# Kernel optimization log

Hardware: AMD Instinct MI355X
Metric: run time of the kernel (lower is better)

The kernel has to match this reference:

```python
import jax, jax.numpy as jnp
import numpy as np

# --- Mamba2Simple hyperparams (from module defaults + headdim=64 hardcode) ---
D_MODEL = 512
D_STATE = 128
EXPAND = 2
HEADDIM = 64
D_INNER = EXPAND * D_MODEL          # 1024
NHEADS = D_INNER // HEADDIM         # 16
NGROUPS = 1
D_CONV = 4
CHUNK = 128                          # SSD chunk length
CONV_DIM = D_INNER + 2 * NGROUPS * D_STATE          # 1280
D_IN_PROJ = 2 * D_INNER + 2 * NGROUPS * D_STATE + NHEADS  # 2320
B_SZ, SEQ = 4, 4096
EPS = 1e-5


def setup_inputs() -> dict:
    key = jax.random.key(0)
    ks = jax.random.split(key, 8)
    x = jax.random.normal(ks[0], (B_SZ, SEQ, D_MODEL), jnp.float32)
    W_in = jax.random.normal(ks[1], (D_IN_PROJ, D_MODEL), jnp.float32) * 0.02
    conv_w = jax.random.normal(ks[2], (CONV_DIM, D_CONV), jnp.float32) * 0.1
    conv_b = jnp.zeros((CONV_DIM,), jnp.float32)
    # dt_bias = inverse-softplus of dt in [1e-3, 0.1] (mamba2 init)
    dt = jax.random.uniform(ks[3], (NHEADS,), jnp.float32, 1e-3, 0.1)
    dt_bias = jnp.log(jnp.expm1(dt))
    A_log = jnp.log(jax.random.uniform(ks[4], (NHEADS,), jnp.float32, 1.0, 16.0))
    D = jnp.ones((NHEADS,), jnp.float32)
    norm_w = jnp.ones((D_INNER,), jnp.float32)
    W_out = jax.random.normal(ks[5], (D_MODEL, D_INNER), jnp.float32) * 0.02
    return dict(x=x, W_in=W_in, conv_w=conv_w, conv_b=conv_b, dt_bias=dt_bias,
                A_log=A_log, D=D, norm_w=norm_w, W_out=W_out)


def _causal_conv(x, w, b):
    """Depthwise causal conv1d. x: (b,l,c), w: (c,K), b: (c,)."""
    lhs = x.transpose(0, 2, 1)          # (b,c,l)
    rhs = w[:, None, :]                  # (c,1,K) depthwise
    out = jax.lax.conv_general_dilated(lhs, rhs, (1,), [(D_CONV - 1, 0)],
                                       feature_group_count=CONV_DIM)
    return out.transpose(0, 2, 1) + b


def _segsum(a):
    """a: (..., T) -> (..., T, T) with out[i,j] = sum_{j<k<=i} a[k], -inf above diag."""
    T = a.shape[-1]
    cs = jnp.cumsum(a, -1)
    seg = cs[..., :, None] - cs[..., None, :]
    mask = jnp.tril(jnp.ones((T, T), bool))
    return jnp.where(mask, seg, -jnp.inf)


def _ssd(X, A, B, C):
    """Chunked SSD scan (ssd_minimal_discrete).
    X: (b,l,h,p) (= dt*x), A: (b,l,h) (= dt*A, negative), B,C: (b,l,n). ngroups=1.
    """
    b, l, h, p = X.shape
    c = l // CHUNK
    Xc = X.reshape(b, c, CHUNK, h, p)
    Ac = A.reshape(b, c, CHUNK, h).transpose(0, 3, 1, 2)   # (b,h,c,q)
    Bc = B.reshape(b, c, CHUNK, -1)                         # (b,c,q,n)
    Cc = C.reshape(b, c, CHUNK, -1)
    A_cs = jnp.cumsum(Ac, -1)                               # (b,h,c,q)
    # intra-chunk (quadratic) part
    Lmat = jnp.exp(_segsum(Ac))                             # (b,h,c,q,q) causal decay
    Y_diag = jnp.einsum('bcqn,bcsn,bhcqs,bcshp->bcqhp', Cc, Bc, Lmat, Xc)
    # per-chunk final states
    decay_states = jnp.exp(A_cs[..., -1:] - A_cs)           # (b,h,c,q)
    states = jnp.einsum('bcqn,bhcq,bcqhp->bchpn', Bc, decay_states, Xc)
    # inter-chunk recurrence (initial state = 0)
    A_last = jnp.pad(A_cs[..., -1], ((0, 0), (0, 0), (1, 0)))  # (b,h,c+1)
    decay_chunk = jnp.exp(_segsum(A_last))                     # (b,h,c+1,c+1)
    states = jnp.concatenate([jnp.zeros_like(states[:, :1]), states], axis=1)
    new_states = jnp.einsum('bhzc,bchpn->bzhpn', decay_chunk, states)
    prev_states = new_states[:, :-1]                           # (b,c,h,p,n)
    Y_off = jnp.einsum('bcqn,bchpn,bhcq->bcqhp', Cc, prev_states, jnp.exp(A_cs))
    return (Y_diag + Y_off).reshape(b, l, h, p)


def _forward(x, W_in, conv_w, conv_b, dt_bias, A_log, D, norm_w, W_out):
    bsz, L, _ = x.shape
    zxbcdt = x @ W_in.T                                   # (b,l,2320)
    z = zxbcdt[..., :D_INNER]
    xBC = zxbcdt[..., D_INNER:D_INNER + CONV_DIM]
    dt = jax.nn.softplus(zxbcdt[..., -NHEADS:] + dt_bias)  # (b,l,h)
    xBC = jax.nn.silu(_causal_conv(xBC, conv_w, conv_b))
    xs = xBC[..., :D_INNER].reshape(bsz, L, NHEADS, HEADDIM)
    Bm = xBC[..., D_INNER:D_INNER + D_STATE]               # (b,l,n)
    Cm = xBC[..., D_INNER + D_STATE:]                      # (b,l,n)
    A = -jnp.exp(A_log)                                    # (h,)
    y = _ssd(xs * dt[..., None], dt * A, Bm, Cm)           # (b,l,h,p)
    y = y + D[None, None, :, None] * xs                    # D skip
    y = y.reshape(bsz, L, D_INNER)
    # gated RMSNorm (norm_before_gate=False): rmsnorm(y * silu(z)) * w
    g = y * jax.nn.silu(z)
    g = g * jax.lax.rsqrt(jnp.mean(g * g, -1, keepdims=True) + EPS) * norm_w
    return x + g @ W_out.T                                 # residual add


def reference(x, W_in, conv_w, conv_b, dt_bias, A_log, D, norm_w, W_out):
    return _forward(x, W_in, conv_w, conv_b, dt_bias, A_log, D, norm_w, W_out)
```

## Files before the change

kernel.cpp:

```cpp
#include <hip/hip_runtime.h>
#include <hip/hip_bf16.h>

typedef __hip_bfloat16 bf16;
typedef __attribute__((ext_vector_type(8))) __bf16 bf16x8;
typedef __attribute__((ext_vector_type(4))) float f32x4;

constexpr int BSZ = 4, SEQ = 4096, DMODEL = 512;
constexpr int DSTATE = 128, HEADDIM = 64, DINNER = 1024, NHEADS = 16, CHUNK = 128;
constexpr int CONVDIM = DINNER + 2 * DSTATE;
constexpr int DINPROJ = 2 * DINNER + 2 * DSTATE + NHEADS;
constexpr int NPAD = 2432;
constexpr int MTOT = BSZ * SEQ;
constexpr int NCHUNK = SEQ / CHUNK;

constexpr size_t OFF_Z    = 0;
constexpr size_t OFF_XBC  = OFF_Z    + (size_t)MTOT * DINNER * 2;
constexpr size_t OFF_DT   = OFF_XBC  + (size_t)MTOT * CONVDIM * 2;
constexpr size_t OFF_XS   = OFF_DT   + (size_t)MTOT * NHEADS * 4;
constexpr size_t OFF_B    = OFF_XS   + (size_t)MTOT * DINNER * 2;
constexpr size_t OFF_C    = OFF_B    + (size_t)MTOT * DSTATE * 2;
constexpr size_t OFF_G    = OFF_C    + (size_t)MTOT * DSTATE * 2;
constexpr size_t OFF_ASUM = OFF_G    + (size_t)BSZ * NCHUNK * CHUNK * CHUNK * 2;
constexpr size_t WS_NEED  = OFF_ASUM + 8192;

static __device__ __forceinline__ float sigmoidf_(float x) { return 1.f / (1.f + __expf(-x)); }
static __device__ __forceinline__ unsigned short f2bf_bits(float f) {
    __hip_bfloat16 h = __float2bfloat16(f);
    return *reinterpret_cast<unsigned short*>(&h);
}
static __device__ __forceinline__ float bfbits2f(unsigned short u) {
    return __bfloat162float(*reinterpret_cast<bf16*>(&u));
}
struct us4 { unsigned short a, b, c, d; };
static __device__ __forceinline__ us4 pack4(const f32x4 v) {
    return { f2bf_bits(v[0]), f2bf_bits(v[1]), f2bf_bits(v[2]), f2bf_bits(v[3]) };
}

__global__ void k_sentinel(float* out) { out[0] = 1.0e9f; }

__global__ __launch_bounds__(256) void k_cast_x(const float* __restrict__ in, bf16* __restrict__ out, int n4) {
    int i = blockIdx.x * 256 + threadIdx.x;
    if (i >= n4) return;
    float4 f = ((const float4*)in)[i];
    us4 v = { f2bf_bits(f.x), f2bf_bits(f.y), f2bf_bits(f.z), f2bf_bits(f.w) };
    ((us4*)out)[i] = v;
}

__global__ __launch_bounds__(256) void k_cast_win(const float* __restrict__ W, bf16* __restrict__ out) {
    int i = blockIdx.x * 256 + threadIdx.x;
    if (i >= NPAD * (DMODEL / 4)) return;
    int row = i / (DMODEL / 4);
    us4 v;
    if (row < DINPROJ) {
        float4 f = ((const float4*)W)[i];
        v = { f2bf_bits(f.x), f2bf_bits(f.y), f2bf_bits(f.z), f2bf_bits(f.w) };
    } else {
        v = { 0, 0, 0, 0 };
    }
    ((us4*)out)[i] = v;
}

typedef const __attribute__((address_space(1))) void* gas_t;
typedef __attribute__((address_space(3))) void* las_t;
static __device__ __forceinline__ void gload_lds16(const void* g, void* l) {
    __builtin_amdgcn_global_load_lds((gas_t)g, (las_t)l, 16, 0, 0);
}

template<int K>
static __device__ __forceinline__ void gemm_core(
    const bf16* __restrict__ A, const bf16* __restrict__ B,
    int m0, int n0, bf16* ldsA, bf16* ldsB, f32x4 acc[4][4])
{
    constexpr int NT = K / 32;
    const int tid = threadIdx.x;
    const int l = tid & 63, w = tid >> 6;
    const int wr = w >> 1, wc = w & 1;
    const int lq = l & 15, lk = l >> 4;

    auto stage = [&](int buf, int t) {
        const int k0 = t * 32;
        #pragma unroll
        for (int i = 0; i < 2; ++i) {
            int q = w * 16 + i * 8 + (l >> 3);
            int p = l & 7;
            int L = p ^ (q & 7);
            int ra = (L >> 2) * 64 + q;
            int ck = L & 3;
            gload_lds16(A + (size_t)(m0 + ra) * K + k0 + ck * 8,
                        ldsA + buf * 4096 + (w * 16 + i * 8) * 64);
            gload_lds16(B + (size_t)(n0 + ra) * K + k0 + ck * 8,
                        ldsB + buf * 4096 + (w * 16 + i * 8) * 64);
        }
    };

    stage(0, 0);
    stage(1, 1);
    for (int t = 0; t < NT; ++t) {
        if (t + 1 < NT) asm volatile("s_waitcnt vmcnt(4)" ::: "memory");
        else            asm volatile("s_waitcnt vmcnt(0)" ::: "memory");
        __builtin_amdgcn_s_barrier();
        __builtin_amdgcn_sched_barrier(0);
        if (t + 2 < NT) stage((t + 2) % 3, t + 2);
        const int buf = t % 3;
        bf16x8 av[4], bv[4];
        #pragma unroll
        for (int f = 0; f < 4; ++f) {
            int ra = wr * 64 + f * 16 + lq;
            int qa = ra & 63, La = (ra >> 6) * 4 + lk, pa = La ^ (qa & 7);
            av[f] = *(const bf16x8*)(ldsA + buf * 4096 + qa * 64 + pa * 8);
            int rb = wc * 64 + f * 16 + lq;
            int qb = rb & 63, Lb = (rb >> 6) * 4 + lk, pb = Lb ^ (qb & 7);
            bv[f] = *(const bf16x8*)(ldsB + buf * 4096 + qb * 64 + pb * 8);
        }
        #pragma unroll
        for (int nf = 0; nf < 4; ++nf)
            #pragma unroll
            for (int mf = 0; mf < 4; ++mf)
                acc[nf][mf] = __builtin_amdgcn_mfma_f32_16x16x32_bf16(bv[nf], av[mf], acc[nf][mf], 0, 0, 0);
    }
}

static __device__ __forceinline__ void swz_block(int& bx, int& by) {
    int gx = gridDim.x;
    int nwg = gx * gridDim.y;
    int wg = by * gx + bx;
    int q = nwg >> 3;
    wg = (wg & 7) * q + (wg >> 3);
    bx = wg % gx; by = wg / gx;
}

__global__ __launch_bounds__(256) void k_gemm_in(
    const bf16* __restrict__ xb, const bf16* __restrict__ Wb,
    const float* __restrict__ dt_bias,
    bf16* __restrict__ z, bf16* __restrict__ xbc, float* __restrict__ dtb)
{
    __shared__ bf16 ldsA[3 * 4096];
    __shared__ bf16 ldsB[3 * 4096];
    int bx = blockIdx.x, by = blockIdx.y;
    swz_block(bx, by);
    const int m0 = by * 128, n0 = bx * 128;
    f32x4 acc[4][4] = {};
    gemm_core<DMODEL>(xb, Wb, m0, n0, ldsA, ldsB, acc);
    const int l = threadIdx.x & 63, w = threadIdx.x >> 6;
    const int wr = w >> 1, wc = w & 1, lq = l & 15, lk = l >> 4;
    const int mg = m0 + wr * 64, ng = n0 + wc * 64;
    if (n0 < DINNER) {
        #pragma unroll
        for (int nf = 0; nf < 4; ++nf)
            #pragma unroll
            for (int mf = 0; mf < 4; ++mf) {
                int n = ng + nf * 16 + lk * 4;
                int m = mg + mf * 16 + lq;
                *(us4*)(z + (size_t)m * DINNER + n) = pack4(acc[nf][mf]);
            }
    } else if (n0 < DINNER + CONVDIM) {
        #pragma unroll
        for (int nf = 0; nf < 4; ++nf)
            #pragma unroll
            for (int mf = 0; mf < 4; ++mf) {
                int n = ng + nf * 16 + lk * 4 - DINNER;
                int m = mg + mf * 16 + lq;
                *(us4*)(xbc + (size_t)m * CONVDIM + n) = pack4(acc[nf][mf]);
            }
    } else {
        #pragma unroll
        for (int nf = 0; nf < 4; ++nf)
            #pragma unroll
            for (int mf = 0; mf < 4; ++mf)
                #pragma unroll
                for (int j = 0; j < 4; ++j) {
                    int n = ng + nf * 16 + lk * 4 + j;
                    int m = mg + mf * 16 + lq;
                    if (n < DINPROJ) {
                        int h = n - (DINNER + CONVDIM);
                        float t = acc[nf][mf][j] + dt_bias[h];
                        dtb[(size_t)m * NHEADS + h] = (t > 20.f) ? t : log1pf(__expf(t));
                    }
                }
    }
}

__global__ __launch_bounds__(256) void k_gemm_out(
    const bf16* __restrict__ gb, const bf16* __restrict__ Wb,
    const float* __restrict__ xres, float* __restrict__ outp)
{
    __shared__ bf16 ldsA[3 * 4096];
    __shared__ bf16 ldsB[3 * 4096];
    int bx = blockIdx.x, by = blockIdx.y;
    swz_block(bx, by);
    const int m0 = by * 128, n0 = bx * 128;
    f32x4 acc[4][4] = {};
    gemm_core<DINNER>(gb, Wb, m0, n0, ldsA, ldsB, acc);
    const int l = threadIdx.x & 63, w = threadIdx.x >> 6;
    const int wr = w >> 1, wc = w & 1, lq = l & 15, lk = l >> 4;
    const int mg = m0 + wr * 64, ng = n0 + wc * 64;
    #pragma unroll
    for (int nf = 0; nf < 4; ++nf)
        #pragma unroll
        for (int mf = 0; mf < 4; ++mf) {
            int n = ng + nf * 16 + lk * 4;
            int m = mg + mf * 16 + lq;
            float4 r = *(const float4*)(xres + (size_t)m * DMODEL + n);
            float4 o = { r.x + acc[nf][mf][0], r.y + acc[nf][mf][1],
                         r.z + acc[nf][mf][2], r.w + acc[nf][mf][3] };
            *(float4*)(outp + (size_t)m * DMODEL + n) = o;
        }
}

constexpr int CTOK = 8;
__global__ __launch_bounds__(320) void k_conv(
    const bf16* __restrict__ xbc, const float* __restrict__ cw, const float* __restrict__ cb,
    bf16* __restrict__ xs, bf16* __restrict__ Bm, bf16* __restrict__ Cm)
{
    const int m0 = blockIdx.x * CTOK;
    const int c4 = threadIdx.x;
    const int c = c4 * 4;
    const int l0 = m0 & 4095;
    float4 cbv = ((const float4*)cb)[c4];
    const float4 w0 = ((const float4*)cw)[c + 0];
    const float4 w1 = ((const float4*)cw)[c + 1];
    const float4 w2 = ((const float4*)cw)[c + 2];
    const float4 w3 = ((const float4*)cw)[c + 3];
    us4 rows[CTOK + 3];
    #pragma unroll
    for (int t = -3; t < CTOK; ++t) {
        int ll = l0 + t;
        if (ll >= 0) rows[t + 3] = *(const us4*)(xbc + (size_t)(m0 + t) * CONVDIM + c);
        else         rows[t + 3] = { 0, 0, 0, 0 };
    }
    #pragma unroll
    for (int t = 0; t < CTOK; ++t) {
        float a0 = cbv.x, a1 = cbv.y, a2 = cbv.z, a3 = cbv.w;
        #pragma unroll
        for (int k = 0; k < 4; ++k) {
            us4 v = rows[t + k];
            a0 += bfbits2f(v.a) * ((const float*)&w0)[k];
            a1 += bfbits2f(v.b) * ((const float*)&w1)[k];
            a2 += bfbits2f(v.c) * ((const float*)&w2)[k];
            a3 += bfbits2f(v.d) * ((const float*)&w3)[k];
        }
        us4 o = { f2bf_bits(a0 * sigmoidf_(a0)), f2bf_bits(a1 * sigmoidf_(a1)),
                  f2bf_bits(a2 * sigmoidf_(a2)), f2bf_bits(a3 * sigmoidf_(a3)) };
        int m = m0 + t;
        if (c < DINNER)               *(us4*)(xs + (size_t)m * DINNER + c) = o;
        else if (c < DINNER + DSTATE) *(us4*)(Bm + (size_t)m * DSTATE + (c - DINNER)) = o;
        else                          *(us4*)(Cm + (size_t)m * DSTATE + (c - DINNER - DSTATE)) = o;
    }
}

__global__ __launch_bounds__(64) void k_gmat(
    const bf16* __restrict__ Cm, const bf16* __restrict__ Bm, bf16* __restrict__ G)
{
    const int bc = blockIdx.z;
    const int q0 = blockIdx.x * 64, s0 = blockIdx.y * 64;
    const int row0 = bc * CHUNK;
    const int l = threadIdx.x;
    const int lq = l & 15, lk = l >> 4;
    f32x4 acc[4][4] = {};
    #pragma unroll
    for (int kc = 0; kc < 4; ++kc) {
        bf16x8 av[4], bv[4];
        #pragma unroll
        for (int f = 0; f < 4; ++f) {
            av[f] = *(const bf16x8*)(Cm + (size_t)(row0 + q0 + f * 16 + lq) * DSTATE + kc * 32 + lk * 8);
            bv[f] = *(const bf16x8*)(Bm + (size_t)(row0 + s0 + f * 16 + lq) * DSTATE + kc * 32 + lk * 8);
        }
        #pragma unroll
        for (int fs = 0; fs < 4; ++fs)
            #pragma unroll
            for (int fq = 0; fq < 4; ++fq)
                acc[fs][fq] = __builtin_amdgcn_mfma_f32_16x16x32_bf16(bv[fs], av[fq], acc[fs][fq], 0, 0, 0);
    }
    #pragma unroll
    for (int fs = 0; fs < 4; ++fs)
        #pragma unroll
        for (int fq = 0; fq < 4; ++fq) {
            int q = q0 + fq * 16 + lq;
            int s = s0 + fs * 16 + lk * 4;
            *(us4*)(G + ((size_t)bc * CHUNK + q) * CHUNK + s) = pack4(acc[fs][fq]);
        }
}

__global__ __launch_bounds__(256) void k_ssd(
    const bf16* __restrict__ xs , const bf16* __restrict__ Bm,
    const float* __restrict__ dtb, const float* __restrict__ A_log,
    const float* __restrict__ Dp, const bf16* __restrict__ G,
    bf16* __restrict__ y, bf16* __restrict__ states, float* __restrict__ asum)
{
    const int h = blockIdx.x, c = blockIdx.y, b = blockIdx.z;
    const int tid = threadIdx.x;
    const int l = tid & 63, w = tid >> 6;
    const int lq = l & 15, lk = l >> 4;
    __shared__ float sa[CHUNK], sdt[CHUNK], sdec[CHUNK];
    __shared__ __bf16 Xt[HEADDIM][136];
    __shared__ __bf16 Bt[DSTATE][136];
    const int row0 = b * SEQ + c * CHUNK;
    const int bc = b * NCHUNK + c;
    const float Ah = -__expf(A_log[h]);
    const float Dh = Dp[h];
    if (tid < CHUNK) {
        float d = dtb[(size_t)(row0 + tid) * NHEADS + h];
        sdt[tid] = d;
        sa[tid] = d * Ah;
    }
    __syncthreads();
    for (int off = 1; off < CHUNK; off <<= 1) {
        float v = 0.f;
        if (tid < CHUNK && tid >= off) v = sa[tid - off];
        __syncthreads();
        if (tid < CHUNK) sa[tid] += v;
        __syncthreads();
    }
    const float alast = sa[CHUNK - 1];
    if (tid < CHUNK) sdec[tid] = __expf(alast - sa[tid]);
    __syncthreads();
    {
        const int s = tid >> 1;
        const float dts = sdt[s];
        #pragma unroll
        for (int li = 0; li < 4; ++li) {
            int p0 = (tid & 1) * 8 + li * 16;
            bf16x8 v = *(const bf16x8*)(xs + (size_t)(row0 + s) * DINNER + h * HEADDIM + p0);
            #pragma unroll
            for (int i = 0; i < 8; ++i) Xt[p0 + i][s] = (__bf16)((float)v[i] * dts);
        }
        #pragma unroll
        for (int li = 0; li < 8; ++li) {
            int n0 = (tid & 1) * 8 + li * 16;
            bf16x8 v = *(const bf16x8*)(Bm + (size_t)(row0 + s) * DSTATE + n0);
            #pragma unroll
            for (int i = 0; i < 8; ++i) Bt[n0 + i][s] = v[i];
        }
    }
    __syncthreads();
    __builtin_amdgcn_s_setprio(1);
    {
        const int q0 = w * 32;
        f32x4 acc[4][2] = {};
        #pragma unroll
        for (int kc = 0; kc < 4; ++kc) {
            const int sbase = kc * 32 + lk * 8;
            bf16x8 av[2];
            #pragma unroll
            for (int fr = 0; fr < 2; ++fr) {
                int q = q0 + fr * 16 + lq;
                bf16x8 g = *(const bf16x8*)(G + ((size_t)bc * CHUNK + q) * CHUNK + sbase);
                float saq = sa[q];
                bf16x8 wv;
                #pragma unroll
                for (int j = 0; j < 8; ++j) {
                    int s = sbase + j;
                    float val = (s <= q) ? __expf(saq - sa[s]) * (float)g[j] : 0.f;
                    wv[j] = (__bf16)val;
                }
                av[fr] = wv;
            }
            #pragma unroll
            for (int pf = 0; pf < 4; ++pf) {
                bf16x8 xv = *(const bf16x8*)&Xt[pf * 16 + lq][sbase];
                #pragma unroll
                for (int fr = 0; fr < 2; ++fr)
                    acc[pf][fr] = __builtin_amdgcn_mfma_f32_16x16x32_bf16(xv, av[fr], acc[pf][fr], 0, 0, 0);
            }
        }
        #pragma unroll
        for (int fr = 0; fr < 2; ++fr)
            #pragma unroll
            for (int pf = 0; pf < 4; ++pf) {
                int q = q0 + fr * 16 + lq;
                int p = pf * 16 + lk * 4;
                size_t idx = (size_t)(row0 + q) * DINNER + h * HEADDIM + p;
                us4 xv4 = *(const us4*)(xs + idx);
                f32x4 a = acc[pf][fr];
                us4 o = { f2bf_bits(a[0] + Dh * bfbits2f(xv4.a)),
                          f2bf_bits(a[1] + Dh * bfbits2f(xv4.b)),
                          f2bf_bits(a[2] + Dh * bfbits2f(xv4.c)),
                          f2bf_bits(a[3] + Dh * bfbits2f(xv4.d)) };
                *(us4*)(y + idx) = o;
            }
    }
    {
        const int n0 = w * 32;
        f32x4 acc[2][4] = {};
        #pragma unroll
        for (int kc = 0; kc < 4; ++kc) {
            const int sbase = kc * 32 + lk * 8;
            bf16x8 xd[4];
            #pragma unroll
            for (int pf = 0; pf < 4; ++pf) {
                bf16x8 xv = *(const bf16x8*)&Xt[pf * 16 + lq][sbase];
                bf16x8 sc;
                #pragma unroll
                for (int j = 0; j < 8; ++j) sc[j] = (__bf16)((float)xv[j] * sdec[sbase + j]);
                xd[pf] = sc;
            }
            #pragma unroll
            for (int nf = 0; nf < 2; ++nf) {
                bf16x8 bb = *(const bf16x8*)&Bt[n0 + nf * 16 + lq][sbase];
                #pragma unroll
                for (int pf = 0; pf < 4; ++pf)
                    acc[nf][pf] = __builtin_amdgcn_mfma_f32_16x16x32_bf16(bb, xd[pf], acc[nf][pf], 0, 0, 0);
            }
        }
        __builtin_amdgcn_s_setprio(0);
        const size_t sb = ((size_t)bc * NHEADS + h) * (HEADDIM * DSTATE);
        #pragma unroll
        for (int nf = 0; nf < 2; ++nf)
            #pragma unroll
            for (int pf = 0; pf < 4; ++pf) {
                int p = pf * 16 + lq;
                int n = n0 + nf * 16 + lk * 4;
                *(us4*)(states + sb + (size_t)p * DSTATE + n) = pack4(acc[nf][pf]);
            }
    }
    if (tid == 0) asum[bc * NHEADS + h] = alast;
}

__global__ __launch_bounds__(256) void k_scan(bf16* __restrict__ states, const float* __restrict__ asum)
{
    const int h = blockIdx.x, b = blockIdx.y, seg = blockIdx.z;
    const int e0 = seg * 512 + threadIdx.x;
    float P[2];
    P[0] = 0.f; P[1] = 0.f;
    for (int c = 0; c < NCHUNK; ++c) {
        size_t base = ((size_t)(b * NCHUNK + c) * NHEADS + h) * (HEADDIM * DSTATE);
        float dec = __expf(asum[(b * NCHUNK + c) * NHEADS + h]);
        #pragma unroll
        for (int j = 0; j < 2; ++j) {
            size_t e = base + e0 + j * 256;
            float sc = __bfloat162float(states[e]);
            states[e] = __float2bfloat16(P[j]);
            P[j] = dec * P[j] + sc;
        }
    }
}

__global__ __launch_bounds__(256) void k_yoff(
    const bf16* __restrict__ Cm,
    const float* __restrict__ dtb, const float* __restrict__ A_log,
    const bf16* __restrict__ states,
    bf16* __restrict__ y)
{
    const int h = blockIdx.x, c = blockIdx.y, b = blockIdx.z;
    const int tid = threadIdx.x;
    const int l = tid & 63, w = tid >> 6;
    const int lq = l & 15, lk = l >> 4;
    __shared__ float sa[CHUNK];
    const int row0 = b * SEQ + c * CHUNK;
    const int bc = b * NCHUNK + c;
    const float Ah = -__expf(A_log[h]);
    if (tid < CHUNK) {
        float d = dtb[(size_t)(row0 + tid) * NHEADS + h];
        sa[tid] = d * Ah;
    }
    __syncthreads();
    for (int off = 1; off < CHUNK; off <<= 1) {
        float v = 0.f;
        if (tid < CHUNK && tid >= off) v = sa[tid - off];
        __syncthreads();
        if (tid < CHUNK) sa[tid] += v;
        __syncthreads();
    }
    const size_t sb = ((size_t)bc * NHEADS + h) * (HEADDIM * DSTATE);
    const int q0 = w * 32;
    f32x4 acc[4][2] = {};
    #pragma unroll
    for (int kc = 0; kc < 4; ++kc) {
        const int nbase = kc * 32 + lk * 8;
        bf16x8 av[2], bv[4];
        #pragma unroll
        for (int fr = 0; fr < 2; ++fr)
            av[fr] = *(const bf16x8*)(Cm + (size_t)(row0 + q0 + fr * 16 + lq) * DSTATE + nbase);
        #pragma unroll
        for (int fc = 0; fc < 4; ++fc)
            bv[fc] = *(const bf16x8*)(states + sb + (size_t)(fc * 16 + lq) * DSTATE + nbase);
        #pragma unroll
        for (int fc = 0; fc < 4; ++fc)
            #pragma unroll
            for (int fr = 0; fr < 2; ++fr)
                acc[fc][fr] = __builtin_amdgcn_mfma_f32_16x16x32_bf16(bv[fc], av[fr], acc[fc][fr], 0, 0, 0);
    }
    #pragma unroll
    for (int fr = 0; fr < 2; ++fr)
        #pragma unroll
        for (int fc = 0; fc < 4; ++fc) {
            int q = q0 + fr * 16 + lq;
            int p = fc * 16 + lk * 4;
            size_t idx = (size_t)(row0 + q) * DINNER + h * HEADDIM + p;
            const float eq = __expf(sa[q]);
            us4 cur = *(const us4*)(y + idx);
            f32x4 a = acc[fc][fr];
            us4 o = { f2bf_bits(bfbits2f(cur.a) + eq * a[0]),
                      f2bf_bits(bfbits2f(cur.b) + eq * a[1]),
                      f2bf_bits(bfbits2f(cur.c) + eq * a[2]),
                      f2bf_bits(bfbits2f(cur.d) + eq * a[3]) };
            *(us4*)(y + idx) = o;
        }
}

__global__ __launch_bounds__(256) void k_norm(
    const bf16* __restrict__ y, const bf16* __restrict__ z,
    const float* __restrict__ norm_w, bf16* __restrict__ g)
{
    const int tid = threadIdx.x;
    const int tk = tid >> 7;
    const int lane = tid & 127;
    const int m = blockIdx.x * 2 + tk;
    const int e0 = lane * 8;
    bf16x8 z8 = *(const bf16x8*)(z + (size_t)m * DINNER + e0);
    bf16x8 y8 = *(const bf16x8*)(y + (size_t)m * DINNER + e0);
    float gg[8];
    float ss = 0.f;
    #pragma unroll
    for (int i = 0; i < 8; ++i) {
        float zz = (float)z8[i];
        gg[i] = (float)y8[i] * (zz * sigmoidf_(zz));
        ss += gg[i] * gg[i];
    }
    #pragma unroll
    for (int o = 32; o > 0; o >>= 1) ss += __shfl_xor(ss, o, 64);
    __shared__ float red[4];
    if ((tid & 63) == 0) red[tid >> 6] = ss;
    __syncthreads();
    const float scale = rsqrtf((red[tk * 2] + red[tk * 2 + 1]) / DINNER + 1e-5f);
    const float4 nw0 = *(const float4*)(norm_w + e0);
    const float4 nw1 = *(const float4*)(norm_w + e0 + 4);
    bf16x8 o8;
    o8[0] = (__bf16)(gg[0] * scale * nw0.x);
    o8[1] = (__bf16)(gg[1] * scale * nw0.y);
    o8[2] = (__bf16)(gg[2] * scale * nw0.z);
    o8[3] = (__bf16)(gg[3] * scale * nw0.w);
    o8[4] = (__bf16)(gg[4] * scale * nw1.x);
    o8[5] = (__bf16)(gg[5] * scale * nw1.y);
    o8[6] = (__bf16)(gg[6] * scale * nw1.z);
    o8[7] = (__bf16)(gg[7] * scale * nw1.w);
    *(bf16x8*)(g + (size_t)m * DINNER + e0) = o8;
}

extern "C" void kernel_launch(void* const* d_in, const int* in_sizes, int n_in,
                              void* d_out, int out_size, void* d_ws, size_t ws_size,
                              hipStream_t stream) {
    const float* x       = (const float*)d_in[0];
    const float* W_in    = (const float*)d_in[1];
    const float* conv_w  = (const float*)d_in[2];
    const float* conv_b  = (const float*)d_in[3];
    const float* dt_bias = (const float*)d_in[4];
    const float* A_log   = (const float*)d_in[5];
    const float* Dp      = (const float*)d_in[6];
    const float* norm_w  = (const float*)d_in[7];
    const float* W_out   = (const float*)d_in[8];
    float* out = (float*)d_out;

    if (ws_size < WS_NEED) {
        k_sentinel<<<1, 1, 0, stream>>>(out);
        return;
    }

    char* ws = (char*)d_ws;
    bf16* z     = (bf16*)(ws + OFF_Z);
    bf16* gb    = (bf16*)(ws + OFF_Z);
    bf16* xbc   = (bf16*)(ws + OFF_XBC);
    bf16* st    = (bf16*)(ws + OFF_XBC);
    float* dtb  = (float*)(ws + OFF_DT);
    bf16* xs    = (bf16*)(ws + OFF_XS);
    bf16* yb    = (bf16*)(ws + OFF_XS);
    bf16* xb    = (bf16*)(ws + OFF_XS);
    bf16* Bm    = (bf16*)(ws + OFF_B);
    bf16* Wbin  = (bf16*)(ws + OFF_B);
    bf16* Cm    = (bf16*)(ws + OFF_C);
    bf16* G     = (bf16*)(ws + OFF_G);
    bf16* Wbout = (bf16*)(ws + OFF_G);
    float* asum = (float*)(ws + OFF_ASUM);

    k_cast_x<<<(MTOT * DMODEL / 4 + 255) / 256, 256, 0, stream>>>(x, xb, MTOT * DMODEL / 4);
    k_cast_win<<<(NPAD * DMODEL / 4 + 255) / 256, 256, 0, stream>>>(W_in, Wbin);
    k_gemm_in<<<dim3(NPAD / 128, MTOT / 128), 256, 0, stream>>>(xb, Wbin, dt_bias, z, xbc, dtb);
    k_conv<<<MTOT / CTOK, 320, 0, stream>>>(xbc, conv_w, conv_b, xs, Bm, Cm);
    k_gmat<<<dim3(2, 2, BSZ * NCHUNK), 64, 0, stream>>>(Cm, Bm, G);
    k_ssd<<<dim3(NHEADS, NCHUNK, BSZ), 256, 0, stream>>>(xs, Bm, dtb, A_log, Dp, G, yb, st, asum);
    k_cast_x<<<(DMODEL * DINNER / 4 + 255) / 256, 256, 0, stream>>>(W_out, Wbout, DMODEL * DINNER / 4);
    k_scan<<<dim3(NHEADS, BSZ, 16), 256, 0, stream>>>(st, asum);
    k_yoff<<<dim3(NHEADS, NCHUNK, BSZ), 256, 0, stream>>>(Cm, dtb, A_log, st, yb);
    k_norm<<<MTOT / 2, 256, 0, stream>>>(yb, z, norm_w, gb);
    k_gemm_out<<<dim3(DMODEL / 128, MTOT / 128), 256, 0, stream>>>(gb, Wbout, x, out);
}
```

Measured before the change: 265.2 us.

## Fuse front casts, enlarge conv token tile, and prefetch in state scan

Merges the x and W_in bf16 cast kernels into one launch to cut launch overhead. Doubles the tokens per conv block, which amortises the halo loads and weight setup over more rows. Restructures the inter-chunk state scan so the next chunk's states and decay are loaded ahead of the current update, hiding the serial load latency. The larger conv tile increases register use per thread and halves the block count.

```diff
diff --git a/kernel.cpp b/kernel.cpp
--- a/kernel.cpp
+++ b/kernel.cpp
@@ -38,25 +38,37 @@
 
 __global__ void k_sentinel(float* out) { out[0] = 1.0e9f; }
 
+constexpr int NX4 = MTOT * DMODEL / 4;
+constexpr int NW4 = NPAD * (DMODEL / 4);
+__global__ __launch_bounds__(256) void k_cast_front(
+    const float* __restrict__ x, const float* __restrict__ W,
+    bf16* __restrict__ xb, bf16* __restrict__ Wb)
+{
+    int i = blockIdx.x * 256 + threadIdx.x;
+    if (i < NX4) {
+        float4 f = ((const float4*)x)[i];
+        us4 v = { f2bf_bits(f.x), f2bf_bits(f.y), f2bf_bits(f.z), f2bf_bits(f.w) };
+        ((us4*)xb)[i] = v;
+    } else {
+        int j = i - NX4;
+        if (j >= NW4) return;
+        int row = j / (DMODEL / 4);
+        us4 v;
+        if (row < DINPROJ) {
+            float4 f = ((const float4*)W)[j];
+            v = { f2bf_bits(f.x), f2bf_bits(f.y), f2bf_bits(f.z), f2bf_bits(f.w) };
+        } else {
+            v = { 0, 0, 0, 0 };
+        }
+        ((us4*)Wb)[j] = v;
+    }
+}
+
 __global__ __launch_bounds__(256) void k_cast_x(const float* __restrict__ in, bf16* __restrict__ out, int n4) {
     int i = blockIdx.x * 256 + threadIdx.x;
     if (i >= n4) return;
     float4 f = ((const float4*)in)[i];
     us4 v = { f2bf_bits(f.x), f2bf_bits(f.y), f2bf_bits(f.z), f2bf_bits(f.w) };
-    ((us4*)out)[i] = v;
-}
-
-__global__ __launch_bounds__(256) void k_cast_win(const float* __restrict__ W, bf16* __restrict__ out) {
-    int i = blockIdx.x * 256 + threadIdx.x;
-    if (i >= NPAD * (DMODEL / 4)) return;
-    int row = i / (DMODEL / 4);
-    us4 v;
-    if (row < DINPROJ) {
-        float4 f = ((const float4*)W)[i];
-        v = { f2bf_bits(f.x), f2bf_bits(f.y), f2bf_bits(f.z), f2bf_bits(f.w) };
-    } else {
-        v = { 0, 0, 0, 0 };
-    }
     ((us4*)out)[i] = v;
 }
 
@@ -207,7 +219,7 @@
         }
 }
 
-constexpr int CTOK = 8;
+constexpr int CTOK = 16;
 __global__ __launch_bounds__(320) void k_conv(
     const bf16* __restrict__ xbc, const float* __restrict__ cw, const float* __restrict__ cb,
     bf16* __restrict__ xs, bf16* __restrict__ Bm, bf16* __restrict__ Cm)
@@ -420,18 +432,26 @@
 {
     const int h = blockIdx.x, b = blockIdx.y, seg = blockIdx.z;
     const int e0 = seg * 512 + threadIdx.x;
-    float P[2];
-    P[0] = 0.f; P[1] = 0.f;
+    constexpr size_t CSTRIDE = (size_t)NHEADS * (HEADDIM * DSTATE);
+    const size_t base = ((size_t)(b * NCHUNK) * NHEADS + h) * (HEADDIM * DSTATE);
+    float P0 = 0.f, P1 = 0.f;
+    bf16 c0 = states[base + e0];
+    bf16 c1 = states[base + e0 + 256];
+    float dec = __expf(asum[(b * NCHUNK) * NHEADS + h]);
     for (int c = 0; c < NCHUNK; ++c) {
-        size_t base = ((size_t)(b * NCHUNK + c) * NHEADS + h) * (HEADDIM * DSTATE);
-        float dec = __expf(asum[(b * NCHUNK + c) * NHEADS + h]);
-        #pragma unroll
-        for (int j = 0; j < 2; ++j) {
-            size_t e = base + e0 + j * 256;
-            float sc = __bfloat162float(states[e]);
-            states[e] = __float2bfloat16(P[j]);
-            P[j] = dec * P[j] + sc;
-        }
+        const size_t cur = base + (size_t)c * CSTRIDE;
+        bf16 n0, n1; float decn = dec;
+        if (c + 1 < NCHUNK) {
+            n0 = states[cur + CSTRIDE + e0];
+            n1 = states[cur + CSTRIDE + e0 + 256];
+            decn = __expf(asum[(b * NCHUNK + c + 1) * NHEADS + h]);
+        }
+        float s0 = __bfloat162float(c0), s1 = __bfloat162float(c1);
+        states[cur + e0]       = __float2bfloat16(P0);
+        states[cur + e0 + 256] = __float2bfloat16(P1);
+        P0 = dec * P0 + s0;
+        P1 = dec * P1 + s1;
+        c0 = n0; c1 = n1; dec = decn;
     }
 }
 
@@ -572,8 +592,7 @@
     bf16* Wbout = (bf16*)(ws + OFF_G);
     float* asum = (float*)(ws + OFF_ASUM);
 
-    k_cast_x<<<(MTOT * DMODEL / 4 + 255) / 256, 256, 0, stream>>>(x, xb, MTOT * DMODEL / 4);
-    k_cast_win<<<(NPAD * DMODEL / 4 + 255) / 256, 256, 0, stream>>>(W_in, Wbin);
+    k_cast_front<<<(NX4 + NW4 + 255) / 256, 256, 0, stream>>>(x, W_in, xb, Wbin);
     k_gemm_in<<<dim3(NPAD / 128, MTOT / 128), 256, 0, stream>>>(xb, Wbin, dt_bias, z, xbc, dtb);
     k_conv<<<MTOT / CTOK, 320, 0, stream>>>(xbc, conv_w, conv_b, xs, Bm, Cm);
     k_gmat<<<dim3(2, 2, BSZ * NCHUNK), 64, 0, stream>>>(Cm, Bm, G);
```

Measured after the change: 268.5 us. No clear change (+1.3%).
